# Kernel optimization log

Hardware: AMD Instinct MI355X
Metric: run time of the kernel (lower is better)

## Reference

```python
import jax, jax.numpy as jnp
import numpy as np

N_NODES = 100000
N_EDGES = 1600000
N_GRAPHS = 2048
NF = 64            # n_filters
N_INTER = 2        # n_interactions
U_MAX = 5.0
STEP = 0.1
GAMMA = 10.0
NG = 51            # number of gaussian rbf centers: arange(0, 5.0+step, 0.1)
LOG2 = float(np.log(2.0))


def ssp(x):
    # shifted softplus (SSPlus)
    return jax.nn.softplus(x) - LOG2


def _lin(key, fan_in, shape):
    return (jax.random.normal(key, shape) / np.sqrt(fan_in)).astype(jnp.float32)


def setup_inputs() -> dict:
    key = jax.random.key(0)
    ks = jax.random.split(key, 40)
    inp = {}
    inp['pos'] = jax.random.normal(ks[0], (N_NODES, 3), dtype=jnp.float32)
    inp['edge_index'] = jax.random.randint(ks[1], (2, N_EDGES), 0, N_NODES)
    inp['z'] = jax.random.randint(ks[2], (N_NODES,), 0, 100)
    inp['batch'] = jnp.sort(jax.random.randint(ks[3], (N_NODES,), 0, N_GRAPHS))
    inp['solvent'] = jax.random.randint(ks[4], (N_GRAPHS,), 0, 4)
    # embeddings (padding_idx=0 for atomic-number embedding)
    inp['emb_z'] = jax.random.normal(ks[5], (100, NF), dtype=jnp.float32).at[0].set(0.0)
    inp['emb_solv'] = jax.random.normal(ks[6], (4, 64), dtype=jnp.float32)
    # mlp_solv: 64 -> 64 -> 32
    inp['solv_w1'] = _lin(ks[7], 64, (64, 64)); inp['solv_b1'] = jnp.zeros((64,), jnp.float32)
    inp['solv_w2'] = _lin(ks[8], 64, (64, 32)); inp['solv_b2'] = jnp.zeros((32,), jnp.float32)
    # per-interaction params stacked over N_INTER
    inp['lin1_w'] = _lin(ks[9], NF, (N_INTER, NF, NF)); inp['lin1_b'] = jnp.zeros((N_INTER, NF), jnp.float32)
    inp['mlp_w1'] = _lin(ks[10], NF, (N_INTER, NF, NF)); inp['mlp_b1'] = jnp.zeros((N_INTER, NF), jnp.float32)
    inp['mlp_w2'] = _lin(ks[11], NF, (N_INTER, NF, NF)); inp['mlp_b2'] = jnp.zeros((N_INTER, NF), jnp.float32)
    inp['filt_w1'] = _lin(ks[12], NG, (N_INTER, NG, NF)); inp['filt_b1'] = jnp.zeros((N_INTER, NF), jnp.float32)
    inp['filt_w2'] = _lin(ks[13], NF, (N_INTER, NF, NF)); inp['filt_b2'] = jnp.zeros((N_INTER, NF), jnp.float32)
    # post_mlp: 64 -> 64 -> 64
    inp['post_w1'] = _lin(ks[14], NF, (NF, NF)); inp['post_b1'] = jnp.zeros((NF,), jnp.float32)
    inp['post_w2'] = _lin(ks[15], NF, (NF, 64)); inp['post_b2'] = jnp.zeros((64,), jnp.float32)
    # post_mlp2: 96 -> 128 -> 32 -> 1
    inp['post2_w1'] = _lin(ks[16], 96, (96, 128)); inp['post2_b1'] = jnp.zeros((128,), jnp.float32)
    inp['post2_w2'] = _lin(ks[17], 128, (128, 32)); inp['post2_b2'] = jnp.zeros((32,), jnp.float32)
    inp['post2_w3'] = _lin(ks[18], 32, (32, 1)); inp['post2_b3'] = jnp.zeros((1,), jnp.float32)
    return inp


def reference(pos, edge_index, z, batch, solvent,
              emb_z, emb_solv, solv_w1, solv_b1, solv_w2, solv_b2,
              lin1_w, lin1_b, mlp_w1, mlp_b1, mlp_w2, mlp_b2,
              filt_w1, filt_b1, filt_w2, filt_b2,
              post_w1, post_b1, post_w2, post_b2,
              post2_w1, post2_b1, post2_w2, post2_b2, post2_w3, post2_b3):
    n_nodes = pos.shape[0]
    n_graphs = solvent.shape[0]
    src, tgt = edge_index[0], edge_index[1]

    # node / solvent embeddings
    x = emb_z[z]                                            # [N, NF]
    s = emb_solv[solvent]                                   # [G, 64]
    s = ssp(s @ solv_w1 + solv_b1) @ solv_w2 + solv_b2      # [G, 32]

    # gaussian rbf expansion of edge distances (computed once, reused per block)
    centers = jnp.arange(0.0, U_MAX + STEP / 2, STEP, dtype=jnp.float32)  # [NG]
    d = jnp.linalg.norm(pos[src] - pos[tgt], axis=-1)       # [E]
    rbf = jnp.exp(-GAMMA * (d[:, None] - centers) ** 2)     # [E, NG]

    for i in range(N_INTER):
        m = x @ lin1_w[i] + lin1_b[i]                       # [N, NF]
        # CFConv filter network on rbf
        W = ssp(rbf @ filt_w1[i] + filt_b1[i]) @ filt_w2[i] + filt_b2[i]  # [E, NF]
        msg = m[src] * W                                    # gather + modulate
        agg = jax.ops.segment_sum(msg, tgt, num_segments=n_nodes)        # scatter-sum
        v = ssp(agg @ mlp_w1[i] + mlp_b1[i]) @ mlp_w2[i] + mlp_b2[i]
        x = x + v                                           # residual

    h = ssp(x @ post_w1 + post_b1) @ post_w2 + post_b2      # [N, 64]
    # scatter-mean pooling over graphs
    counts = jax.ops.segment_sum(jnp.ones((n_nodes,), h.dtype), batch, num_segments=n_graphs)
    pooled = jax.ops.segment_sum(h, batch, num_segments=n_graphs) / jnp.maximum(counts, 1.0)[:, None]

    out = jnp.concatenate([pooled, s], axis=1)              # [G, 96]
    out = ssp(out @ post2_w1 + post2_b1)
    out = ssp(out @ post2_w2 + post2_b2)
    out = out @ post2_w3 + post2_b3                         # [G, 1]
    return out
```

## Files before the change

### kernel.cpp

```cpp
#include <hip/hip_runtime.h>
#include <hip/hip_bf16.h>
#include <hip/hip_fp16.h>

#define TABN   4096
#define ROWS   (TABN + 1)
#define DMAX   6.5f
#define DELTA  (DMAX / (float)TABN)
#define INVD   ((float)TABN / DMAX)
#define LOG2F_ 0.6931471805599453f
#define SBITS  9
#define TILE   2048

__device__ __forceinline__ float ssp(float x) {
    return fmaxf(x, 0.f) + __logf(1.f + __expf(-fabsf(x))) - LOG2F_;
}

__global__ void ftab_kernel(const float* __restrict__ fw1, const float* __restrict__ fb1,
                            const float* __restrict__ fw2, const float* __restrict__ fb2,
                            float* __restrict__ ftab) {
    int t = blockIdx.x;
    int i = blockIdx.y;
    int j = threadIdx.x;
    float d = (float)t * DELTA;
    float acc = fb1[i * 64 + j];
    for (int k = 0; k < 51; ++k) {
        float u = d - 0.1f * (float)k;
        float r = __expf(-10.f * u * u);
        acc = fmaf(r, fw1[((size_t)i * 51 + k) * 64 + j], acc);
    }
    __shared__ float h[64];
    h[j] = ssp(acc);
    __syncthreads();
    float o = fb2[i * 64 + j];
    for (int k = 0; k < 64; ++k)
        o = fmaf(h[k], fw2[((size_t)i * 64 + k) * 64 + j], o);
    ftab[((size_t)i * ROWS + t) * 64 + j] = o;
}

__global__ void fpack_kernel(const float* __restrict__ ftab, __half2* __restrict__ fpair) {
    int t = blockIdx.x, i = blockIdx.y, j = threadIdx.x;
    const float* r = ftab + ((size_t)i * ROWS + t) * 64;
    fpair[((size_t)i * TABN + t) * 64 + j] = __floats2half2_rn(r[j], r[j + 64]);
}

__global__ void bhist_kernel(const int* __restrict__ ei, int* __restrict__ bcnt, int E) {
    __shared__ int h[256];
    int tid = threadIdx.x;
    h[tid] = 0;
    __syncthreads();
    for (int e = blockIdx.x * blockDim.x + tid; e < E; e += gridDim.x * blockDim.x)
        atomicAdd(&h[ei[E + e] >> SBITS], 1);
    __syncthreads();
    if (h[tid]) atomicAdd(&bcnt[tid], h[tid]);
}

__global__ void bscan_kernel(const int* __restrict__ bcnt, int* __restrict__ bbase,
                             int* __restrict__ bcur, int nbuck) {
    __shared__ int sm[256];
    int tid = threadIdx.x;
    int v = (tid < nbuck) ? bcnt[tid] : 0;
    sm[tid] = v;
    __syncthreads();
    for (int o = 1; o < 256; o <<= 1) {
        int t = (tid >= o) ? sm[tid - o] : 0;
        __syncthreads();
        sm[tid] += t;
        __syncthreads();
    }
    if (tid < nbuck) { bbase[tid] = sm[tid] - v; bcur[tid] = sm[tid] - v; }
    if (tid == 255) bbase[nbuck] = sm[255];
}

__global__ __launch_bounds__(256, 4)
void stage_kernel(const float* __restrict__ pos, const int* __restrict__ ei,
                  int* __restrict__ bcur, int2* __restrict__ stg, int E, int nbuck) {
    __shared__ int hist[256], loff[256], gbase[256], sc[256];
    __shared__ int2 sp[TILE];
    __shared__ short sb[TILE];
    int tid = threadIdx.x;
    int tile0 = blockIdx.x * TILE;
    int cnt = min(TILE, E - tile0);
    hist[tid] = 0;
    __syncthreads();
    int myrank[8], myb[8]; int2 mypay[8];
#pragma unroll
    for (int u = 0; u < 8; ++u) {
        int i = u * 256 + tid;
        myb[u] = -1;
        if (i < cnt) {
            int e = tile0 + i;
            int s = ei[e], t = ei[E + e];
            float dx = pos[3 * s]     - pos[3 * t];
            float dy = pos[3 * s + 1] - pos[3 * t + 1];
            float dz = pos[3 * s + 2] - pos[3 * t + 2];
            float d = sqrtf(dx * dx + dy * dy + dz * dz);
            float ds = fminf(d, DMAX) * INVD;
            int ti = min((int)ds, TABN - 1);
            int frq = min((int)((ds - (float)ti) * 1048576.f), 1048575);
            mypay[u] = make_int2(s | ((t & 511) << 17), (ti << 20) | frq);
            myb[u] = t >> SBITS;
            myrank[u] = atomicAdd(&hist[myb[u]], 1);
        }
    }
    __syncthreads();
    sc[tid] = hist[tid];
    __syncthreads();
    for (int o = 1; o < 256; o <<= 1) {
        int v = (tid >= o) ? sc[tid - o] : 0;
        __syncthreads();
        sc[tid] += v;
        __syncthreads();
    }
    loff[tid] = sc[tid] - hist[tid];
    if (tid < nbuck && hist[tid] > 0) gbase[tid] = atomicAdd(&bcur[tid], hist[tid]);
    __syncthreads();
#pragma unroll
    for (int u = 0; u < 8; ++u)
        if (myb[u] >= 0) {
            int idx = loff[myb[u]] + myrank[u];
            sp[idx] = mypay[u];
            sb[idx] = (short)myb[u];
        }
    __syncthreads();
    for (int i = tid; i < cnt; i += 256) {
        int b = sb[i];
        stg[gbase[b] + (i - loff[b])] = sp[i];
    }
}

__global__ __launch_bounds__(256)
void place_kernel(const int2* __restrict__ stg, const int* __restrict__ bbase,
                  int* __restrict__ off, int2* __restrict__ edata, int n, int nbuck) {
    int b = blockIdx.x;
    int n0 = b << SBITS;
    int nn = min(512, n - n0);
    int q0 = bbase[b], q1 = bbase[b + 1];
    __shared__ int cnt[512], cur[512], sc[256];
    int tid = threadIdx.x;
    cnt[tid] = 0; cnt[tid + 256] = 0;
    __syncthreads();
    for (int q = q0 + tid; q < q1; q += 256)
        atomicAdd(&cnt[(stg[q].x >> 17) & 511], 1);
    __syncthreads();
    int c0 = cnt[2 * tid], c1 = cnt[2 * tid + 1];
    int s = c0 + c1;
    sc[tid] = s;
    __syncthreads();
    for (int o = 1; o < 256; o <<= 1) {
        int v = (tid >= o) ? sc[tid - o] : 0;
        __syncthreads();
        sc[tid] += v;
        __syncthreads();
    }
    int run = sc[tid] - s;
    cur[2 * tid] = run;
    cur[2 * tid + 1] = run + c0;
    if (2 * tid < nn)     off[n0 + 2 * tid]     = q0 + run;
    if (2 * tid + 1 < nn) off[n0 + 2 * tid + 1] = q0 + run + c0;
    if (b == nbuck - 1 && tid == 0) off[n] = q1;
    __syncthreads();
    for (int q = q0 + tid; q < q1; q += 256) {
        int2 v = stg[q];
        int p = atomicAdd(&cur[(v.x >> 17) & 511], 1);
        edata[q0 + p] = v;
    }
}

__global__ void embed_kernel(const int* __restrict__ z, const float* __restrict__ emb,
                             float* __restrict__ x, int n) {
    int idx = blockIdx.x * blockDim.x + threadIdx.x;
    if (idx >= n * 16) return;
    int node = idx >> 4, c = idx & 15;
    ((float4*)x)[idx] = ((const float4*)emb)[z[node] * 16 + c];
}

__global__ void solv_kernel(const float* __restrict__ emb_solv,
                            const float* __restrict__ w1, const float* __restrict__ b1,
                            const float* __restrict__ w2, const float* __restrict__ b2,
                            float* __restrict__ s4) {
    __shared__ float h[4][64];
    int t = threadIdx.x, r = t >> 6, j = t & 63;
    float acc = b1[j];
    for (int k = 0; k < 64; ++k) acc = fmaf(emb_solv[r * 64 + k], w1[k * 64 + j], acc);
    h[r][j] = ssp(acc);
    __syncthreads();
    if (j < 32) {
        float a = b2[j];
        for (int k = 0; k < 64; ++k) a = fmaf(h[r][k], w2[k * 32 + j], a);
        s4[r * 32 + j] = a;
    }
}

__global__ __launch_bounds__(256, 4)
void mm1h_kernel(const int* __restrict__ z, const float* __restrict__ emb,
                 const float* __restrict__ w, const float* __restrict__ b,
                 __half* __restrict__ out, int n) {
    int tid = threadIdx.x;
    int q = __builtin_amdgcn_readfirstlane(tid >> 6);
    int node = blockIdx.x * 64 + (tid & 63);
    node = min(node, n - 1);
    int zi = z[node];
    const float4* in4 = (const float4*)(emb + (size_t)zi * 64);
    const float* wq = w + q * 16;
    const float* bq = b + q * 16;
    float acc[16];
#pragma unroll
    for (int j = 0; j < 16; ++j) acc[j] = bq[j];
#pragma unroll 2
    for (int kk = 0; kk < 16; ++kk) {
        float4 xv = in4[kk];
        const float* w0 = wq + kk * 256;
#pragma unroll
        for (int j = 0; j < 16; ++j) acc[j] = fmaf(xv.x, w0[j],       acc[j]);
#pragma unroll
        for (int j = 0; j < 16; ++j) acc[j] = fmaf(xv.y, w0[64 + j],  acc[j]);
#pragma unroll
        for (int j = 0; j < 16; ++j) acc[j] = fmaf(xv.z, w0[128 + j], acc[j]);
#pragma unroll
        for (int j = 0; j < 16; ++j) acc[j] = fmaf(xv.w, w0[192 + j], acc[j]);
    }
    __half2* o2 = (__half2*)(out + (size_t)node * 64 + q * 16);
#pragma unroll
    for (int c = 0; c < 8; ++c)
        o2[c] = __floats2half2_rn(acc[2 * c], acc[2 * c + 1]);
}

__global__ void agg_kernel(const int* __restrict__ off, const int2* __restrict__ edata,
                           const __half* __restrict__ m, const __half2* __restrict__ fpair,
                           __half* __restrict__ agg, int n) {
    int wave = (blockIdx.x * blockDim.x + threadIdx.x) >> 6;
    int lane = threadIdx.x & 63;
    if (wave >= n) return;
    int e0 = __builtin_amdgcn_readfirstlane(off[wave]);
    int e1 = __builtin_amdgcn_readfirstlane(off[wave + 1]);
    const float FRS = 1.f / 1048576.f;
    float acc[4] = {0.f, 0.f, 0.f, 0.f};
    int e = e0;
    for (; e + 8 <= e1; e += 8) {
        float mv[8], wv[8];
#pragma unroll
        for (int u = 0; u < 8; ++u) {
            int2 pd = edata[e + u];
            int px = __builtin_amdgcn_readfirstlane(pd.x);
            int py = __builtin_amdgcn_readfirstlane(pd.y);
            int s = px & 0x1FFFF;
            unsigned ti = ((unsigned)py) >> 20;
            float fr = (float)(py & 0xFFFFF) * FRS;
            mv[u] = __half2float(m[(size_t)s * 64 + lane]);
            float2 wf = __half22float2(fpair[(size_t)ti * 64 + lane]);
            wv[u] = fmaf(fr, wf.y - wf.x, wf.x);
        }
#pragma unroll
        for (int u = 0; u < 8; ++u) acc[u & 3] = fmaf(mv[u], wv[u], acc[u & 3]);
    }
    for (; e + 4 <= e1; e += 4) {
        float mv[4], wv[4];
#pragma unroll
        for (int u = 0; u < 4; ++u) {
            int2 pd = edata[e + u];
            int px = __builtin_amdgcn_readfirstlane(pd.x);
            int py = __builtin_amdgcn_readfirstlane(pd.y);
            int s = px & 0x1FFFF;
            unsigned ti = ((unsigned)py) >> 20;
            float fr = (float)(py & 0xFFFFF) * FRS;
            mv[u] = __half2float(m[(size_t)s * 64 + lane]);
            float2 wf = __half22float2(fpair[(size_t)ti * 64 + lane]);
            wv[u] = fmaf(fr, wf.y - wf.x, wf.x);
        }
#pragma unroll
        for (int u = 0; u < 4; ++u) acc[u] = fmaf(mv[u], wv[u], acc[u]);
    }
    for (; e < e1; ++e) {
        int2 pd = edata[e];
        int px = __builtin_amdgcn_readfirstlane(pd.x);
        int py = __builtin_amdgcn_readfirstlane(pd.y);
        int s = px & 0x1FFFF;
        unsigned ti = ((unsigned)py) >> 20;
        float fr = (float)(py & 0xFFFFF) * FRS;
        float mm = __half2float(m[(size_t)s * 64 + lane]);
        float2 wf = __half22float2(fpair[(size_t)ti * 64 + lane]);
        acc[0] = fmaf(mm, fmaf(fr, wf.y - wf.x, wf.x), acc[0]);
    }
    agg[(size_t)wave * 64 + lane] = __float2half((acc[0] + acc[1]) + (acc[2] + acc[3]));
}

#define HSTR 65
template <bool INH, bool RES, bool EMIT_M, bool OUTH>
__global__ __launch_bounds__(256, 4)
void mm2_kernel(const void* __restrict__ in_,
                const float* __restrict__ w1, const float* __restrict__ b1,
                const float* __restrict__ w2, const float* __restrict__ b2,
                const float* __restrict__ res, void* __restrict__ out_,
                const float* __restrict__ lw, const float* __restrict__ lb,
                __half* __restrict__ mout, int n) {
    __shared__ float hl[64 * HSTR];
    int tid = threadIdx.x;
    int q = __builtin_amdgcn_readfirstlane(tid >> 6);
    int nl = tid & 63;
    int node = blockIdx.x * 64 + nl;
    node = min(node, n - 1);

    const float* w1q = w1 + q * 16;
    const float* b1q = b1 + q * 16;
    float acc[16];
#pragma unroll
    for (int j = 0; j < 16; ++j) acc[j] = b1q[j];
    if constexpr (INH) {
        const float4* in4 = (const float4*)((const __half*)in_ + (size_t)node * 64);
#pragma unroll 1
        for (int kk = 0; kk < 8; ++kk) {
            float4 raw = in4[kk];
            const __half2* hp = (const __half2*)&raw;
            float xs[8];
#pragma unroll
            for (int p = 0; p < 4; ++p) {
                float2 f = __half22float2(hp[p]);
                xs[2 * p] = f.x; xs[2 * p + 1] = f.y;
            }
#pragma unroll
            for (int r = 0; r < 8; ++r) {
                const float* w0 = w1q + (kk * 8 + r) * 64;
#pragma unroll
                for (int j = 0; j < 16; ++j) acc[j] = fmaf(xs[r], w0[j], acc[j]);
            }
        }
    } else {
        const float4* in4 = (const float4*)((const float*)in_ + (size_t)node * 64);
#pragma unroll 2
        for (int kk = 0; kk < 16; ++kk) {
            float4 xv = in4[kk];
            const float* w0 = w1q + kk * 256;
#pragma unroll
            for (int j = 0; j < 16; ++j) acc[j] = fmaf(xv.x, w0[j],       acc[j]);
#pragma unroll
            for (int j = 0; j < 16; ++j) acc[j] = fmaf(xv.y, w0[64 + j],  acc[j]);
#pragma unroll
            for (int j = 0; j < 16; ++j) acc[j] = fmaf(xv.z, w0[128 + j], acc[j]);
#pragma unroll
            for (int j = 0; j < 16; ++j) acc[j] = fmaf(xv.w, w0[192 + j], acc[j]);
        }
    }
    float* hrow = hl + nl * HSTR + q * 16;
#pragma unroll
    for (int j = 0; j < 16; ++j) hrow[j] = ssp(acc[j]);
    __syncthreads();

    const float* hfull = hl + nl * HSTR;
    const float* w2q = w2 + q * 16;
    const float* b2q = b2 + q * 16;
    float acc2[16];
#pragma unroll
    for (int j = 0; j < 16; ++j) acc2[j] = b2q[j];
#pragma unroll 8
    for (int k = 0; k < 64; ++k) {
        float hk = hfull[k];
        const float* w0 = w2q + k * 64;
#pragma unroll
        for (int j = 0; j < 16; ++j) acc2[j] = fmaf(hk, w0[j], acc2[j]);
    }
    if constexpr (RES) {
        const float4* r4 = (const float4*)(res + (size_t)node * 64 + q * 16);
#pragma unroll
        for (int c = 0; c < 4; ++c) {
            float4 rv = r4[c];
            acc2[4 * c]     += rv.x; acc2[4 * c + 1] += rv.y;
            acc2[4 * c + 2] += rv.z; acc2[4 * c + 3] += rv.w;
        }
    }
    if constexpr (OUTH) {
        __half2* o2 = (__half2*)((__half*)out_ + (size_t)node * 64 + q * 16);
#pragma unroll
        for (int c = 0; c < 8; ++c)
            o2[c] = __floats2half2_rn(acc2[2 * c], acc2[2 * c + 1]);
    } else {
        float4* o4 = (float4*)((float*)out_ + (size_t)node * 64 + q * 16);
#pragma unroll
        for (int c = 0; c < 4; ++c)
            o4[c] = make_float4(acc2[4 * c], acc2[4 * c + 1],
                                acc2[4 * c + 2], acc2[4 * c + 3]);
    }
    if constexpr (EMIT_M) {
        __syncthreads();
#pragma unroll
        for (int j = 0; j < 16; ++j) hrow[j] = acc2[j];
        __syncthreads();
        const float* lwq = lw + q * 16;
        float accm[16];
#pragma unroll
        for (int j = 0; j < 16; ++j) accm[j] = lb[q * 16 + j];
#pragma unroll 8
        for (int k = 0; k < 64; ++k) {
            float hk = hfull[k];
            const float* w0 = lwq + k * 64;
#pragma unroll
            for (int j = 0; j < 16; ++j) accm[j] = fmaf(hk, w0[j], accm[j]);
        }
        __half2* o2 = (__half2*)(mout + (size_t)node * 64 + q * 16);
#pragma unroll
        for (int c = 0; c < 8; ++c)
            o2[c] = __floats2half2_rn(accm[2 * c], accm[2 * c + 1]);
    }
}

__global__ void pool_kernel(const __half* __restrict__ h, const int* __restrict__ batch,
                            float* __restrict__ pooled, int n_nodes) {
    int g = blockIdx.x, j = threadIdx.x;
    int lo = 0, hi = n_nodes;
    while (lo < hi) { int mid = (lo + hi) >> 1; if (batch[mid] < g) lo = mid + 1; else hi = mid; }
    int start = lo;
    int lo2 = start, hi2 = n_nodes;
    while (lo2 < hi2) { int mid = (lo2 + hi2) >> 1; if (batch[mid] < g + 1) lo2 = mid + 1; else hi2 = mid; }
    int end = lo2;
    float acc = 0.f;
    for (int r = start; r < end; ++r) acc += __half2float(h[(size_t)r * 64 + j]);
    float cnt = (float)(end - start);
    pooled[(size_t)g * 64 + j] = acc / fmaxf(cnt, 1.f);
}

__global__ void post2_kernel(const float* __restrict__ pooled, const float* __restrict__ s4,
                             const int* __restrict__ solvent,
                             const float* __restrict__ w1, const float* __restrict__ b1,
                             const float* __restrict__ w2, const float* __restrict__ b2,
                             const float* __restrict__ w3, const float* __restrict__ b3,
                             float* __restrict__ out) {
    __shared__ float in96[96];
    __shared__ float l1[128];
    __shared__ float l2[32];
    int g = blockIdx.x, t = threadIdx.x;
    if (t < 64)      in96[t] = pooled[(size_t)g * 64 + t];
    else if (t < 96) in96[t] = s4[solvent[g] * 32 + (t - 64)];
    __syncthreads();
    float acc = b1[t];
    for (int k = 0; k < 96; ++k) acc = fmaf(in96[k], w1[k * 128 + t], acc);
    l1[t] = ssp(acc);
    __syncthreads();
    if (t < 32) {
        float a = b2[t];
        for (int k = 0; k < 128; ++k) a = fmaf(l1[k], w2[k * 32 + t], a);
        l2[t] = ssp(a);
    }
    __syncthreads();
    if (t < 32) {
        float p = l2[t] * w3[t];
        for (int o = 16; o >= 1; o >>= 1) p += __shfl_down(p, o);
        if (t == 0) out[g] = p + b3[0];
    }
}

extern "C" void kernel_launch(void* const* d_in, const int* in_sizes, int n_in,
                              void* d_out, int out_size, void* d_ws, size_t ws_size,
                              hipStream_t stream) {
    const float* pos      = (const float*)d_in[0];
    const int*   ei       = (const int*)d_in[1];
    const int*   z        = (const int*)d_in[2];
    const int*   batch    = (const int*)d_in[3];
    const int*   solvent  = (const int*)d_in[4];
    const float* emb_z    = (const float*)d_in[5];
    const float* emb_solv = (const float*)d_in[6];
    const float* solv_w1  = (const float*)d_in[7];  const float* solv_b1 = (const float*)d_in[8];
    const float* solv_w2  = (const float*)d_in[9];  const float* solv_b2 = (const float*)d_in[10];
    const float* lin1_w   = (const float*)d_in[11]; const float* lin1_b  = (const float*)d_in[12];
    const float* mlp_w1   = (const float*)d_in[13]; const float* mlp_b1  = (const float*)d_in[14];
    const float* mlp_w2   = (const float*)d_in[15]; const float* mlp_b2  = (const float*)d_in[16];
    const float* filt_w1  = (const float*)d_in[17]; const float* filt_b1 = (const float*)d_in[18];
    const float* filt_w2  = (const float*)d_in[19]; const float* filt_b2 = (const float*)d_in[20];
    const float* post_w1  = (const float*)d_in[21]; const float* post_b1 = (const float*)d_in[22];
    const float* post_w2  = (const float*)d_in[23]; const float* post_b2 = (const float*)d_in[24];
    const float* p2w1 = (const float*)d_in[25]; const float* p2b1 = (const float*)d_in[26];
    const float* p2w2 = (const float*)d_in[27]; const float* p2b2 = (const float*)d_in[28];
    const float* p2w3 = (const float*)d_in[29]; const float* p2b3 = (const float*)d_in[30];
    float* out = (float*)d_out;

    const int N = in_sizes[2];
    const int E = in_sizes[1] / 2;
    const int G = in_sizes[4];
    const int NBUCK = (N + (1 << SBITS) - 1) >> SBITS;

    char* wp = (char*)d_ws;
    auto alloc = [&](size_t bytes) -> void* {
        void* r = (void*)wp;
        wp += (bytes + 255) & ~(size_t)255;
        return r;
    };
    int2*    stg    = (int2*)   alloc((size_t)E * 8);
    int2*    edata  = (int2*)   alloc((size_t)E * 8);
    int*     bcnt   = (int*)    alloc(256 * 4);
    int*     bbase  = (int*)    alloc(257 * 4);
    int*     bcur   = (int*)    alloc(256 * 4);
    int*     off    = (int*)    alloc((size_t)(N + 1) * 4);
    float*   ftab   = (float*)  alloc((size_t)2 * ROWS * 64 * 4);
    __half2* fpair  = (__half2*)alloc((size_t)2 * TABN * 64 * 4);
    float*   s4     = (float*)  alloc(4 * 32 * 4);
    float*   x      = (float*)  alloc((size_t)N * 64 * 4);
    __half*  m_h    = (__half*) alloc((size_t)N * 64 * 2);
    __half*  m_h2   = (__half*) alloc((size_t)N * 64 * 2);
    __half*  agg_h  = (__half*) alloc((size_t)N * 64 * 2);
    __half*  hbuf   = (__half*) alloc((size_t)N * 64 * 2);
    float*   pooled = (float*)  alloc((size_t)G * 64 * 4);
    (void)ws_size; (void)n_in; (void)out_size;

    hipMemsetAsync(bcnt, 0, 256 * 4, stream);

    ftab_kernel<<<dim3(ROWS, 2), 64, 0, stream>>>(filt_w1, filt_b1, filt_w2, filt_b2, ftab);
    fpack_kernel<<<dim3(TABN, 2), 64, 0, stream>>>(ftab, fpair);
    bhist_kernel<<<512, 256, 0, stream>>>(ei, bcnt, E);
    bscan_kernel<<<1, 256, 0, stream>>>(bcnt, bbase, bcur, NBUCK);
    stage_kernel<<<(E + TILE - 1) / TILE, 256, 0, stream>>>(pos, ei, bcur, stg, E, NBUCK);
    place_kernel<<<NBUCK, 256, 0, stream>>>(stg, bbase, off, edata, N, NBUCK);
    embed_kernel<<<((size_t)N * 16 + 255) / 256, 256, 0, stream>>>(z, emb_z, x, N);
    solv_kernel<<<1, 256, 0, stream>>>(emb_solv, solv_w1, solv_b1, solv_w2, solv_b2, s4);

    int mmg = (N + 63) / 64;
    mm1h_kernel<<<mmg, 256, 0, stream>>>(z, emb_z, lin1_w, lin1_b, m_h, N);
    agg_kernel<<<(N + 3) / 4, 256, 0, stream>>>(off, edata, m_h, fpair, agg_h, N);
    mm2_kernel<true, true, true, false><<<mmg, 256, 0, stream>>>(
        agg_h, mlp_w1, mlp_b1, mlp_w2, mlp_b2, x, x,
        lin1_w + 4096, lin1_b + 64, m_h2, N);
    agg_kernel<<<(N + 3) / 4, 256, 0, stream>>>(off, edata, m_h2,
                                                fpair + (size_t)TABN * 64, agg_h, N);
    mm2_kernel<true, true, false, false><<<mmg, 256, 0, stream>>>(
        agg_h, mlp_w1 + 4096, mlp_b1 + 64, mlp_w2 + 4096, mlp_b2 + 64, x, x,
        nullptr, nullptr, nullptr, N);
    mm2_kernel<false, false, false, true><<<mmg, 256, 0, stream>>>(
        x, post_w1, post_b1, post_w2, post_b2, nullptr, hbuf,
        nullptr, nullptr, nullptr, N);

    pool_kernel<<<G, 64, 0, stream>>>(hbuf, batch, pooled, N);
    post2_kernel<<<G, 128, 0, stream>>>(pooled, s4, solvent, p2w1, p2b1, p2w2, p2b2,
                                        p2w3, p2b3, out);
}
```

Baseline: 362.9 us.

## Replace scalar-FMA node MLP kernels with fp16 MFMA and store residual x in fp16

Rewrites the per-node two-layer MLP kernels to use 16x16x32 fp16 MFMA instructions on transposed fp16 weights, packed once by a new kernel. The residual state x is now stored in fp16 instead of fp32, which halves its memory traffic. The goal is to cut the scalar FMA cost and bandwidth of the node MLPs. In exchange, precision drops: the hidden activations and the residual accumulation are now rounded to fp16.

```diff
diff --git a/kernel.cpp b/kernel.cpp
--- a/kernel.cpp
+++ b/kernel.cpp
@@ -10,6 +10,9 @@
 #define LOG2F_ 0.6931471805599453f
 #define SBITS  9
 #define TILE   2048
+
+typedef _Float16 f16x8 __attribute__((ext_vector_type(8)));
+typedef float    f32x4 __attribute__((ext_vector_type(4)));
 
 __device__ __forceinline__ float ssp(float x) {
     return fmaxf(x, 0.f) + __logf(1.f + __expf(-fabsf(x))) - LOG2F_;
@@ -41,6 +44,14 @@
     int t = blockIdx.x, i = blockIdx.y, j = threadIdx.x;
     const float* r = ftab + ((size_t)i * ROWS + t) * 64;
     fpair[((size_t)i * TABN + t) * 64 + j] = __floats2half2_rn(r[j], r[j + 64]);
+}
+
+__global__ void wpack_kernel(const float* w0, const float* w1, const float* w2,
+                             const float* w3, const float* w4, const float* w5,
+                             const float* w6, __half* __restrict__ wt) {
+    const float* ws[7] = {w0, w1, w2, w3, w4, w5, w6};
+    int nrow = blockIdx.x, mat = blockIdx.y, k = threadIdx.x;
+    wt[((size_t)mat * 64 + nrow) * 64 + k] = __float2half(ws[mat][k * 64 + nrow]);
 }
 
 __global__ void bhist_kernel(const int* __restrict__ ei, int* __restrict__ bcnt, int E) {
@@ -167,11 +178,17 @@
 }
 
 __global__ void embed_kernel(const int* __restrict__ z, const float* __restrict__ emb,
-                             float* __restrict__ x, int n) {
+                             __half* __restrict__ xh, int n) {
     int idx = blockIdx.x * blockDim.x + threadIdx.x;
-    if (idx >= n * 16) return;
-    int node = idx >> 4, c = idx & 15;
-    ((float4*)x)[idx] = ((const float4*)emb)[z[node] * 16 + c];
+    if (idx >= n * 8) return;
+    int node = idx >> 3, c = idx & 7;
+    const float4* e4 = (const float4*)(emb + (size_t)z[node] * 64 + c * 8);
+    float4 a = e4[0], b = e4[1];
+    __half2* o2 = (__half2*)(xh + (size_t)node * 64 + c * 8);
+    o2[0] = __floats2half2_rn(a.x, a.y);
+    o2[1] = __floats2half2_rn(a.z, a.w);
+    o2[2] = __floats2half2_rn(b.x, b.y);
+    o2[3] = __floats2half2_rn(b.z, b.w);
 }
 
 __global__ void solv_kernel(const float* __restrict__ emb_solv,
@@ -284,121 +301,90 @@
     agg[(size_t)wave * 64 + lane] = __float2half((acc[0] + acc[1]) + (acc[2] + acc[3]));
 }
 
-#define HSTR 65
-template <bool INH, bool RES, bool EMIT_M, bool OUTH>
+template <bool RES, bool EMIT_M>
 __global__ __launch_bounds__(256, 4)
-void mm2_kernel(const void* __restrict__ in_,
-                const float* __restrict__ w1, const float* __restrict__ b1,
-                const float* __restrict__ w2, const float* __restrict__ b2,
-                const float* __restrict__ res, void* __restrict__ out_,
-                const float* __restrict__ lw, const float* __restrict__ lb,
-                __half* __restrict__ mout, int n) {
-    __shared__ float hl[64 * HSTR];
+void mfmlp_kernel(const __half* __restrict__ in,
+                  const __half* __restrict__ w1t, const float* __restrict__ b1,
+                  const __half* __restrict__ w2t, const float* __restrict__ b2,
+                  const __half* __restrict__ res, __half* __restrict__ out,
+                  const __half* __restrict__ lwt, const float* __restrict__ lb,
+                  __half* __restrict__ mout, int n) {
+    __shared__ __half hls[4][16][72];
     int tid = threadIdx.x;
-    int q = __builtin_amdgcn_readfirstlane(tid >> 6);
-    int nl = tid & 63;
-    int node = blockIdx.x * 64 + nl;
-    node = min(node, n - 1);
-
-    const float* w1q = w1 + q * 16;
-    const float* b1q = b1 + q * 16;
-    float acc[16];
-#pragma unroll
-    for (int j = 0; j < 16; ++j) acc[j] = b1q[j];
-    if constexpr (INH) {
-        const float4* in4 = (const float4*)((const __half*)in_ + (size_t)node * 64);
-#pragma unroll 1
-        for (int kk = 0; kk < 8; ++kk) {
-            float4 raw = in4[kk];
-            const __half2* hp = (const __half2*)&raw;
-            float xs[8];
-#pragma unroll
-            for (int p = 0; p < 4; ++p) {
-                float2 f = __half22float2(hp[p]);
-                xs[2 * p] = f.x; xs[2 * p + 1] = f.y;
+    int w = tid >> 6, l = tid & 63;
+    int lm = l & 15, lg = l >> 4;
+    int base = blockIdx.x * 64 + w * 16;
+    int arow = min(base + lm, n - 1);
+
+    f32x4 acc[4];
+#pragma unroll
+    for (int nt = 0; nt < 4; ++nt) acc[nt] = (f32x4){0.f, 0.f, 0.f, 0.f};
+#pragma unroll
+    for (int s = 0; s < 2; ++s) {
+        f16x8 a = *(const f16x8*)(in + (size_t)arow * 64 + 32 * s + 8 * lg);
+#pragma unroll
+        for (int nt = 0; nt < 4; ++nt) {
+            f16x8 b = *(const f16x8*)(w1t + (size_t)(lm + 16 * nt) * 64 + 32 * s + 8 * lg);
+            acc[nt] = __builtin_amdgcn_mfma_f32_16x16x32_f16(a, b, acc[nt], 0, 0, 0);
+        }
+    }
+#pragma unroll
+    for (int nt = 0; nt < 4; ++nt) {
+        float bb = b1[lm + 16 * nt];
+#pragma unroll
+        for (int i = 0; i < 4; ++i)
+            hls[w][lg * 4 + i][lm + 16 * nt] = __float2half(ssp(acc[nt][i] + bb));
+    }
+
+    f32x4 acc2[4];
+#pragma unroll
+    for (int nt = 0; nt < 4; ++nt) acc2[nt] = (f32x4){0.f, 0.f, 0.f, 0.f};
+#pragma unroll
+    for (int s = 0; s < 2; ++s) {
+        f16x8 a = *(const f16x8*)(&hls[w][lm][32 * s + 8 * lg]);
+#pragma unroll
+        for (int nt = 0; nt < 4; ++nt) {
+            f16x8 b = *(const f16x8*)(w2t + (size_t)(lm + 16 * nt) * 64 + 32 * s + 8 * lg);
+            acc2[nt] = __builtin_amdgcn_mfma_f32_16x16x32_f16(a, b, acc2[nt], 0, 0, 0);
+        }
+    }
+#pragma unroll
+    for (int nt = 0; nt < 4; ++nt) {
+        float bb = b2[lm + 16 * nt];
+#pragma unroll
+        for (int i = 0; i < 4; ++i) {
+            int r = base + lg * 4 + i;
+            if (r < n) {
+                float v = acc2[nt][i] + bb;
+                if constexpr (RES) v += __half2float(res[(size_t)r * 64 + lm + 16 * nt]);
+                out[(size_t)r * 64 + lm + 16 * nt] = __float2half(v);
+                if constexpr (EMIT_M) hls[w][lg * 4 + i][lm + 16 * nt] = __float2half(v);
             }
-#pragma unroll
-            for (int r = 0; r < 8; ++r) {
-                const float* w0 = w1q + (kk * 8 + r) * 64;
-#pragma unroll
-                for (int j = 0; j < 16; ++j) acc[j] = fmaf(xs[r], w0[j], acc[j]);
+        }
+    }
+    if constexpr (EMIT_M) {
+        f32x4 acc3[4];
+#pragma unroll
+        for (int nt = 0; nt < 4; ++nt) acc3[nt] = (f32x4){0.f, 0.f, 0.f, 0.f};
+#pragma unroll
+        for (int s = 0; s < 2; ++s) {
+            f16x8 a = *(const f16x8*)(&hls[w][lm][32 * s + 8 * lg]);
+#pragma unroll
+            for (int nt = 0; nt < 4; ++nt) {
+                f16x8 b = *(const f16x8*)(lwt + (size_t)(lm + 16 * nt) * 64 + 32 * s + 8 * lg);
+                acc3[nt] = __builtin_amdgcn_mfma_f32_16x16x32_f16(a, b, acc3[nt], 0, 0, 0);
             }
         }
-    } else {
-        const float4* in4 = (const float4*)((const float*)in_ + (size_t)node * 64);
-#pragma unroll 2
-        for (int kk = 0; kk < 16; ++kk) {
-            float4 xv = in4[kk];
-            const float* w0 = w1q + kk * 256;
-#pragma unroll
-            for (int j = 0; j < 16; ++j) acc[j] = fmaf(xv.x, w0[j],       acc[j]);
-#pragma unroll
-            for (int j = 0; j < 16; ++j) acc[j] = fmaf(xv.y, w0[64 + j],  acc[j]);
-#pragma unroll
-            for (int j = 0; j < 16; ++j) acc[j] = fmaf(xv.z, w0[128 + j], acc[j]);
-#pragma unroll
-            for (int j = 0; j < 16; ++j) acc[j] = fmaf(xv.w, w0[192 + j], acc[j]);
-        }
-    }
-    float* hrow = hl + nl * HSTR + q * 16;
-#pragma unroll
-    for (int j = 0; j < 16; ++j) hrow[j] = ssp(acc[j]);
-    __syncthreads();
-
-    const float* hfull = hl + nl * HSTR;
-    const float* w2q = w2 + q * 16;
-    const float* b2q = b2 + q * 16;
-    float acc2[16];
-#pragma unroll
-    for (int j = 0; j < 16; ++j) acc2[j] = b2q[j];
-#pragma unroll 8
-    for (int k = 0; k < 64; ++k) {
-        float hk = hfull[k];
-        const float* w0 = w2q + k * 64;
-#pragma unroll
-        for (int j = 0; j < 16; ++j) acc2[j] = fmaf(hk, w0[j], acc2[j]);
-    }
-    if constexpr (RES) {
-        const float4* r4 = (const float4*)(res + (size_t)node * 64 + q * 16);
-#pragma unroll
-        for (int c = 0; c < 4; ++c) {
-            float4 rv = r4[c];
-            acc2[4 * c]     += rv.x; acc2[4 * c + 1] += rv.y;
-            acc2[4 * c + 2] += rv.z; acc2[4 * c + 3] += rv.w;
-        }
-    }
-    if constexpr (OUTH) {
-        __half2* o2 = (__half2*)((__half*)out_ + (size_t)node * 64 + q * 16);
-#pragma unroll
-        for (int c = 0; c < 8; ++c)
-            o2[c] = __floats2half2_rn(acc2[2 * c], acc2[2 * c + 1]);
-    } else {
-        float4* o4 = (float4*)((float*)out_ + (size_t)node * 64 + q * 16);
-#pragma unroll
-        for (int c = 0; c < 4; ++c)
-            o4[c] = make_float4(acc2[4 * c], acc2[4 * c + 1],
-                                acc2[4 * c + 2], acc2[4 * c + 3]);
-    }
-    if constexpr (EMIT_M) {
-        __syncthreads();
-#pragma unroll
-        for (int j = 0; j < 16; ++j) hrow[j] = acc2[j];
-        __syncthreads();
-        const float* lwq = lw + q * 16;
-        float accm[16];
-#pragma unroll
-        for (int j = 0; j < 16; ++j) accm[j] = lb[q * 16 + j];
-#pragma unroll 8
-        for (int k = 0; k < 64; ++k) {
-            float hk = hfull[k];
-            const float* w0 = lwq + k * 64;
-#pragma unroll
-            for (int j = 0; j < 16; ++j) accm[j] = fmaf(hk, w0[j], accm[j]);
-        }
-        __half2* o2 = (__half2*)(mout + (size_t)node * 64 + q * 16);
-#pragma unroll
-        for (int c = 0; c < 8; ++c)
-            o2[c] = __floats2half2_rn(accm[2 * c], accm[2 * c + 1]);
+#pragma unroll
+        for (int nt = 0; nt < 4; ++nt) {
+            float bb = lb[lm + 16 * nt];
+#pragma unroll
+            for (int i = 0; i < 4; ++i) {
+                int r = base + lg * 4 + i;
+                if (r < n)
+                    mout[(size_t)r * 64 + lm + 16 * nt] = __float2half(acc3[nt][i] + bb);
+            }
+        }
     }
 }
 
@@ -490,8 +476,9 @@
     int*     off    = (int*)    alloc((size_t)(N + 1) * 4);
     float*   ftab   = (float*)  alloc((size_t)2 * ROWS * 64 * 4);
     __half2* fpair  = (__half2*)alloc((size_t)2 * TABN * 64 * 4);
+    __half*  wt     = (__half*) alloc((size_t)7 * 4096 * 2);
     float*   s4     = (float*)  alloc(4 * 32 * 4);
-    float*   x      = (float*)  alloc((size_t)N * 64 * 4);
+    __half*  x_h    = (__half*) alloc((size_t)N * 64 * 2);
     __half*  m_h    = (__half*) alloc((size_t)N * 64 * 2);
     __half*  m_h2   = (__half*) alloc((size_t)N * 64 * 2);
     __half*  agg_h  = (__half*) alloc((size_t)N * 64 * 2);
@@ -503,26 +490,29 @@
 
     ftab_kernel<<<dim3(ROWS, 2), 64, 0, stream>>>(filt_w1, filt_b1, filt_w2, filt_b2, ftab);
     fpack_kernel<<<dim3(TABN, 2), 64, 0, stream>>>(ftab, fpair);
+    wpack_kernel<<<dim3(64, 7), 64, 0, stream>>>(mlp_w1, mlp_w2, mlp_w1 + 4096,
+                                                 mlp_w2 + 4096, post_w1, post_w2,
+                                                 lin1_w + 4096, wt);
     bhist_kernel<<<512, 256, 0, stream>>>(ei, bcnt, E);
     bscan_kernel<<<1, 256, 0, stream>>>(bcnt, bbase, bcur, NBUCK);
     stage_kernel<<<(E + TILE - 1) / TILE, 256, 0, stream>>>(pos, ei, bcur, stg, E, NBUCK);
     place_kernel<<<NBUCK, 256, 0, stream>>>(stg, bbase, off, edata, N, NBUCK);
-    embed_kernel<<<((size_t)N * 16 + 255) / 256, 256, 0, stream>>>(z, emb_z, x, N);
+    embed_kernel<<<((size_t)N * 8 + 255) / 256, 256, 0, stream>>>(z, emb_z, x_h, N);
     solv_kernel<<<1, 256, 0, stream>>>(emb_solv, solv_w1, solv_b1, solv_w2, solv_b2, s4);
 
     int mmg = (N + 63) / 64;
     mm1h_kernel<<<mmg, 256, 0, stream>>>(z, emb_z, lin1_w, lin1_b, m_h, N);
     agg_kernel<<<(N + 3) / 4, 256, 0, stream>>>(off, edata, m_h, fpair, agg_h, N);
-    mm2_kernel<true, true, true, false><<<mmg, 256, 0, stream>>>(
-        agg_h, mlp_w1, mlp_b1, mlp_w2, mlp_b2, x, x,
-        lin1_w + 4096, lin1_b + 64, m_h2, N);
+    mfmlp_kernel<true, true><<<mmg, 256, 0, stream>>>(
+        agg_h, wt, mlp_b1, wt + 4096, mlp_b2, x_h, x_h,
+        wt + 6 * 4096, lin1_b + 64, m_h2, N);
     agg_kernel<<<(N + 3) / 4, 256, 0, stream>>>(off, edata, m_h2,
                                                 fpair + (size_t)TABN * 64, agg_h, N);
-    mm2_kernel<true, true, false, false><<<mmg, 256, 0, stream>>>(
-        agg_h, mlp_w1 + 4096, mlp_b1 + 64, mlp_w2 + 4096, mlp_b2 + 64, x, x,
+    mfmlp_kernel<true, false><<<mmg, 256, 0, stream>>>(
+        agg_h, wt + 2 * 4096, mlp_b1 + 64, wt + 3 * 4096, mlp_b2 + 64, x_h, x_h,
         nullptr, nullptr, nullptr, N);
-    mm2_kernel<false, false, false, true><<<mmg, 256, 0, stream>>>(
-        x, post_w1, post_b1, post_w2, post_b2, nullptr, hbuf,
+    mfmlp_kernel<false, false><<<mmg, 256, 0, stream>>>(
+        x_h, wt + 4 * 4096, post_b1, wt + 5 * 4096, post_b2, nullptr, hbuf,
         nullptr, nullptr, nullptr, N);
 
     pool_kernel<<<G, 64, 0, stream>>>(hbuf, batch, pooled, N);
```

New measurement: 333.4 us. 8.2% less time.
